# Kernel tuning notes

Hardware: AMD Instinct MI355X
Metric: run time of the kernel (lower is better)

Reference implementation:

```python
import jax, jax.numpy as jnp
import numpy as np
import math

B, L, D = 4, 1024, 1024
H, S = 16, 64
HD = D // H
EPS_LN = 1e-12


def _band_logits_init():
    bl = np.zeros((H, S), dtype=np.float32)
    for h in range(H):
        center = (h + 0.5) * (S / max(H, 1.0))
        for s in range(S):
            dist = s + 0.5 - center
            bl[h, s] = -dist * dist
    return jnp.asarray(bl)


def setup_inputs() -> dict:
    key = jax.random.key(0)
    ks = jax.random.split(key, 12)
    std = 1.0 / math.sqrt(D)
    inp = {
        "hidden_states": jax.random.normal(ks[0], (B, L, D), jnp.float32),
        "attention_mask": jnp.zeros((B, 1, 1, L), jnp.float32),
        "cos_phi": jax.random.normal(ks[1], (B, S, L), jnp.float32),
        "sin_phi": jax.random.normal(ks[2], (B, S, L), jnp.float32),
        "mag": jax.random.uniform(ks[3], (B, S, L), jnp.float32),
        "Wq": jax.random.normal(ks[4], (D, D), jnp.float32) * std,
        "bq": jnp.zeros((D,), jnp.float32),
        "Wk": jax.random.normal(ks[5], (D, D), jnp.float32) * std,
        "bk": jnp.zeros((D,), jnp.float32),
        "Wv": jax.random.normal(ks[6], (D, D), jnp.float32) * std,
        "bv": jnp.zeros((D,), jnp.float32),
        "Wo": jax.random.normal(ks[7], (D, D), jnp.float32) * std,
        "bo": jnp.zeros((D,), jnp.float32),
        "band_logits": _band_logits_init(),
        "phase_bias": jnp.full((H,), 0.5, jnp.float32),
        "gamma": jnp.full((H, S), -3.0, jnp.float32),
        "ln_w": jnp.ones((D,), jnp.float32),
        "ln_b": jnp.zeros((D,), jnp.float32),
    }
    return inp


def _shape_heads(x):
    # [B,L,D] -> [B,H,L,HD]
    return x.reshape(B, L, H, HD).transpose(0, 2, 1, 3)


def reference(hidden_states, attention_mask, cos_phi, sin_phi, mag,
              Wq, bq, Wk, bk, Wv, bv, Wo, bo,
              band_logits, phase_bias, gamma, ln_w, ln_b):
    residual = hidden_states
    q = _shape_heads(hidden_states @ Wq.T + bq)
    k = _shape_heads(hidden_states @ Wk.T + bk)
    v = _shape_heads(hidden_states @ Wv.T + bv)

    cos_pl = cos_phi.transpose(0, 2, 1)  # [B,L,S]
    sin_pl = sin_phi.transpose(0, 2, 1)
    mag_pl = mag.transpose(0, 2, 1)
    mag_pl = mag_pl / (mag_pl.mean(axis=-1, keepdims=True) + 1e-8)

    gamma_pos = jax.nn.softplus(gamma)  # [H,S]
    mag_mix = jnp.tanh(jnp.einsum('bls,hs->bhl', mag_pl, gamma_pos))
    scale = 1.0 + 0.5 * mag_mix[..., None]  # [B,H,L,1]
    q = q * scale
    k = k * scale
    v = v * scale

    attn_scores = jnp.einsum('bhld,bhmd->bhlm', q, k) / math.sqrt(HD)

    band_w_sqrt = jnp.sqrt(jax.nn.softmax(band_logits, axis=-1) + 1e-8)  # [H,S]
    cos_feat = cos_pl[:, None] * band_w_sqrt[None, :, None, :]  # [B,H,L,S]
    sin_feat = sin_pl[:, None] * band_w_sqrt[None, :, None, :]
    phase_align = (jnp.einsum('bhls,bhms->bhlm', cos_feat, cos_feat)
                   + jnp.einsum('bhls,bhms->bhlm', sin_feat, sin_feat)) / math.sqrt(S)

    phase_scale = jax.nn.softplus(phase_bias)[None, :, None, None]
    attn_scores = attn_scores + phase_scale * phase_align + attention_mask

    attn_probs = jax.nn.softmax(attn_scores, axis=-1)
    context = jnp.einsum('bhlm,bhmd->bhld', attn_probs, v)
    context = context.transpose(0, 2, 1, 3).reshape(B, L, D)

    out = context @ Wo.T + bo
    x = out + residual
    mu = x.mean(axis=-1, keepdims=True)
    var = ((x - mu) ** 2).mean(axis=-1, keepdims=True)
    return (x - mu) / jnp.sqrt(var + EPS_LN) * ln_w + ln_b
```

## Files before the change

kernel.cpp:

```cpp
#include <hip/hip_runtime.h>
#include <hip/hip_bf16.h>
#include <math.h>

#define DEV __device__ __forceinline__

typedef __attribute__((ext_vector_type(8))) short short8;
typedef __attribute__((ext_vector_type(8))) unsigned short ushort8v;
typedef __attribute__((ext_vector_type(4))) float f32x4;

DEV unsigned short f2bf(float f) {
  unsigned u = __float_as_uint(f);
  u = u + 0x7fffu + ((u >> 16) & 1u);
  return (unsigned short)(u >> 16);
}

DEV float softplus_f(float x) {
  return (x > 20.f) ? x : log1pf(expf(x));
}

DEV int sw64(int r, int e) { return r * 64 + (e ^ (((r) & 7) << 3)); }
DEV int sw128(int r, int e) { return r * 128 + (e ^ (((r) & 7) << 3)); }

#define GL16(gp, lp) __builtin_amdgcn_global_load_lds( \
    (const __attribute__((address_space(1))) unsigned int*)(gp), \
    (__attribute__((address_space(3))) unsigned int*)(lp), 16, 0, 0)

__global__ __launch_bounds__(256) void k_convall(
    const float* __restrict__ hs, const float* __restrict__ wq,
    const float* __restrict__ wk, const float* __restrict__ wv,
    const float* __restrict__ wo, ushort4* __restrict__ hsb4,
    ushort4* __restrict__ wcat4, ushort4* __restrict__ wob4) {
  const int i = blockIdx.x * 256 + threadIdx.x;
  const float* src;
  ushort4* dst;
  int off;
  if (i < 1048576) {
    src = hs; dst = hsb4; off = i;
  } else {
    const int j = i - 1048576;
    const int g = j >> 18;
    off = j & 262143;
    if (g == 0)      { src = wq; dst = wcat4; }
    else if (g == 1) { src = wk; dst = wcat4 + 262144; }
    else if (g == 2) { src = wv; dst = wcat4 + 524288; }
    else             { src = wo; dst = wob4; }
  }
  const float4 v = reinterpret_cast<const float4*>(src)[off];
  ushort4 o;
  o.x = f2bf(v.x); o.y = f2bf(v.y); o.z = f2bf(v.z); o.w = f2bf(v.w);
  dst[off] = o;
}

__global__ __launch_bounds__(256) void k_prep(
    const float* __restrict__ cos_phi, const float* __restrict__ sin_phi,
    const float* __restrict__ mag, const float* __restrict__ band_logits,
    const float* __restrict__ phase_bias, const float* __restrict__ gamma,
    float* __restrict__ scaleB, unsigned short* __restrict__ feat) {
  const int b = blockIdx.x >> 6;
  const int l0 = ((blockIdx.x >> 2) & 15) << 6;
  const int hq = blockIdx.x & 3;
  const int t = threadIdx.x, lane = t & 63, w = t >> 6;
  __shared__ float cosL[64][65];
  __shared__ float sinL[64][65];
  __shared__ float magL[64][65];
  __shared__ float psum[4][64];
  __shared__ float minv[64];
  __shared__ float bwssL[4][64];
  __shared__ float gposL[4][64];

  {
    const int h = (hq << 2) + w;
    float bl = band_logits[h * 64 + lane];
    float mx = bl;
#pragma unroll
    for (int m = 1; m < 64; m <<= 1) mx = fmaxf(mx, __shfl_xor(mx, m));
    float e = __expf(bl - mx);
    float sm = e;
#pragma unroll
    for (int m = 1; m < 64; m <<= 1) sm += __shfl_xor(sm, m);
    const float ps = softplus_f(phase_bias[h]);
    bwssL[w][lane] = sqrtf(e / sm + 1e-8f) * sqrtf(ps * 0.125f);
    gposL[w][lane] = softplus_f(gamma[h * 64 + lane]);
  }

  const size_t boff = (size_t)b * 65536;
  for (int it = 0; it < 16; ++it) {
    const int s = it * 4 + w, l = lane;
    const size_t g = boff + (size_t)s * 1024 + l0 + l;
    cosL[s][l] = cos_phi[g];
    sinL[s][l] = sin_phi[g];
    magL[s][l] = mag[g];
  }
  __syncthreads();
  {
    const int l = t & 63, g = t >> 6;
    float acc = 0.f;
    for (int i = 0; i < 16; ++i) acc += magL[g * 16 + i][l];
    psum[g][l] = acc;
  }
  __syncthreads();
  if (t < 64) {
    float mean = (psum[0][t] + psum[1][t] + psum[2][t] + psum[3][t]) * (1.f / 64.f);
    minv[t] = 1.f / (mean + 1e-8f);
  }
  __syncthreads();
  {
    const int l = lane;
    const float iv = minv[l];
    const int hidx = (hq << 2) + w;
    float acc = 0.f;
    for (int s = 0; s < 64; ++s) acc += magL[s][l] * gposL[w][s];
    const float tnh = tanhf(acc * iv);
    scaleB[(size_t)(((b << 4) + hidx) << 10) + l0 + l] = 1.f + 0.5f * tnh;
  }
  const int l = t >> 2, sq = (t & 3) << 4;
  for (int hh = 0; hh < 4; ++hh) {
    const int h = (hq << 2) + hh;
    unsigned short* fp = feat + ((size_t)(((b << 4) + h) << 10) + l0 + l) * 128;
    unsigned short cb[16], sb[16];
#pragma unroll
    for (int j = 0; j < 16; ++j) {
      const int s = sq + j;
      const float bw = bwssL[hh][s];
      cb[j] = f2bf(bw * cosL[s][l]);
      sb[j] = f2bf(bw * sinL[s][l]);
    }
    *reinterpret_cast<ushort8v*>(fp + sq) = *reinterpret_cast<ushort8v*>(cb);
    *reinterpret_cast<ushort8v*>(fp + sq + 8) = *reinterpret_cast<ushort8v*>(cb + 8);
    *reinterpret_cast<ushort8v*>(fp + 64 + sq) = *reinterpret_cast<ushort8v*>(sb);
    *reinterpret_cast<ushort8v*>(fp + 64 + sq + 8) = *reinterpret_cast<ushort8v*>(sb + 8);
  }
}

template <int MODE>
__global__ __launch_bounds__(256) void k_gemm(
    const unsigned short* __restrict__ A, const unsigned short* __restrict__ Bt,
    int Ntiles, int K,
    const float* __restrict__ bq, const float* __restrict__ bk,
    const float* __restrict__ bv, const float* __restrict__ scaleB,
    unsigned short* __restrict__ qbuf, unsigned short* __restrict__ kbuf,
    unsigned short* __restrict__ vT,
    const float* __restrict__ bo, const float* __restrict__ resid,
    float* __restrict__ xout) {
  __shared__ __align__(16) short As[128 * 64];
  __shared__ __align__(16) short Bs[128 * 64];
  const int t = threadIdx.x;
  const int lane = t & 63;
  const int w = t >> 6;
  const int cpx = gridDim.x >> 3;
  const int swz = (blockIdx.x & 7) * cpx + (blockIdx.x >> 3);
  const int tm = (swz / Ntiles) << 7;
  const int tn = (swz % Ntiles) << 7;
  const int wR = (w >> 1) << 6;
  const int wC = (w & 1) << 6;
  const int rowS = t >> 3;
  const int offS = (t & 7) << 3;
  const int sgm = (rowS & 7) << 3;
  const int ka = (lane >> 4) << 3;
  const int lm = lane & 15;

  const f32x4 vzero = {0.f, 0.f, 0.f, 0.f};
  f32x4 acc[4][4];
#pragma unroll
  for (int i = 0; i < 4; ++i)
#pragma unroll
    for (int j = 0; j < 4; ++j) acc[i][j] = vzero;

  for (int kt = 0; kt < K; kt += 64) {
    __syncthreads();
#pragma unroll
    for (int p = 0; p < 4; ++p) {
      GL16(A + (size_t)(tm + p * 32 + rowS) * K + kt + (offS ^ sgm), (char*)As + p * 4096 + w * 1024);
      GL16(Bt + (size_t)(tn + p * 32 + rowS) * K + kt + (offS ^ sgm), (char*)Bs + p * 4096 + w * 1024);
    }
    __syncthreads();
    short8 af[4][2], bf[4][2];
#pragma unroll
    for (int mt = 0; mt < 4; ++mt) {
      const int r = wR + mt * 16 + lm;
      af[mt][0] = *(const short8*)&As[sw64(r, ka)];
      af[mt][1] = *(const short8*)&As[sw64(r, 32 + ka)];
    }
#pragma unroll
    for (int nt = 0; nt < 4; ++nt) {
      const int r = wC + nt * 16 + lm;
      bf[nt][0] = *(const short8*)&Bs[sw64(r, ka)];
      bf[nt][1] = *(const short8*)&Bs[sw64(r, 32 + ka)];
    }
#pragma unroll
    for (int mt = 0; mt < 4; ++mt)
#pragma unroll
      for (int nt = 0; nt < 4; ++nt) {
        acc[mt][nt] = __builtin_amdgcn_mfma_f32_16x16x32_bf16(af[mt][0], bf[nt][0], acc[mt][nt], 0, 0, 0);
        acc[mt][nt] = __builtin_amdgcn_mfma_f32_16x16x32_bf16(af[mt][1], bf[nt][1], acc[mt][nt], 0, 0, 0);
      }
  }

#pragma unroll
  for (int mt = 0; mt < 4; ++mt) {
#pragma unroll
    for (int r = 0; r < 4; ++r) {
      const int row = tm + wR + mt * 16 + ((lane >> 4) << 2) + r;
#pragma unroll
      for (int nt = 0; nt < 4; ++nt) {
        const int col = tn + wC + nt * 16 + lm;
        float v = acc[mt][nt][r];
        if (MODE == 0) {
          const int b = row >> 10, l = row & 1023;
          const int sect = col >> 10, jj = col & 1023;
          const int h = jj >> 6, hd = jj & 63;
          const int bh = (b << 4) + h;
          const float sc = scaleB[((size_t)bh << 10) + l];
          if (sect == 0) {
            qbuf[((size_t)bh * 1024 + l) * 64 + hd] = f2bf((v + bq[jj]) * sc * 0.125f);
          } else if (sect == 1) {
            kbuf[((size_t)bh * 1024 + l) * 64 + hd] = f2bf((v + bk[jj]) * sc);
          } else {
            vT[(size_t)bh * 65536 + (size_t)hd * 1024 + l] = f2bf((v + bv[jj]) * sc);
          }
        } else {
          xout[(size_t)row * 1024 + col] = v + bo[col] + resid[(size_t)row * 1024 + col];
        }
      }
    }
  }
}

__global__ __launch_bounds__(256) void k_attn(
    const unsigned short* __restrict__ qbuf, const unsigned short* __restrict__ kbuf,
    const unsigned short* __restrict__ vT, const unsigned short* __restrict__ feat,
    const float* __restrict__ maskg, unsigned short* __restrict__ ctx) {
  __shared__ __align__(16) short Kq[64 * 64];
  __shared__ __align__(16) short Kf[64 * 128];
  __shared__ __align__(16) short Vt[64 * 64];
  __shared__ __align__(16) short Pb[4][16 * 64];

  const int t = threadIdx.x, lane = t & 63, w = t >> 6;
  const int bh = blockIdx.x & 63;
  const int qt = blockIdx.x >> 6;
  const int b = bh >> 4, h = bh & 15;
  const int lm = lane & 15;
  const int ka = (lane >> 4) << 3;

  const int rA = t >> 3, oA = (t & 7) << 3;
  const int rF = t >> 4, oF = (t & 15) << 3;
  const int swA = (rA & 7) << 3;
  const int swF = (rF & 7) << 3;

  const size_t qrow = ((size_t)bh << 10) + qt * 64 + w * 16 + lm;
  short8 aq[2], af[4];
  aq[0] = *(const short8*)(qbuf + qrow * 64 + ka);
  aq[1] = *(const short8*)(qbuf + qrow * 64 + 32 + ka);
#pragma unroll
  for (int kk = 0; kk < 4; ++kk) af[kk] = *(const short8*)(feat + qrow * 128 + kk * 32 + ka);

  short8 ones;
#pragma unroll
  for (int i = 0; i < 8; ++i) ones[i] = (short)0x3F80;

  const f32x4 vzero = {0.f, 0.f, 0.f, 0.f};
  float m_i[4], l_i[4];
  f32x4 o[4];
#pragma unroll
  for (int r = 0; r < 4; ++r) { m_i[r] = -INFINITY; l_i[r] = 0.f; }
#pragma unroll
  for (int nt = 0; nt < 4; ++nt) o[nt] = vzero;

  for (int mt = 0; mt < 16; ++mt) {
    __syncthreads();
#pragma unroll
    for (int p = 0; p < 2; ++p) {
      GL16(kbuf + (((size_t)bh << 10) + mt * 64 + p * 32 + rA) * 64 + (oA ^ swA),
           (char*)Kq + p * 4096 + w * 1024);
      GL16(vT + ((size_t)bh << 16) + (size_t)(p * 32 + rA) * 1024 + mt * 64 + (oA ^ swA),
           (char*)Vt + p * 4096 + w * 1024);
    }
#pragma unroll
    for (int p = 0; p < 4; ++p) {
      GL16(feat + (((size_t)bh << 10) + mt * 64 + p * 16 + rF) * 128 + (oF ^ swF),
           (char*)Kf + p * 4096 + w * 1024);
    }
    float mk[4];
#pragma unroll
    for (int nt = 0; nt < 4; ++nt) mk[nt] = maskg[(b << 10) + mt * 64 + nt * 16 + lm];
    __syncthreads();

    f32x4 s[4];
#pragma unroll
    for (int nt = 0; nt < 4; ++nt) s[nt] = vzero;
#pragma unroll
    for (int nt = 0; nt < 4; ++nt) {
      const int rk = nt * 16 + lm;
      s[nt] = __builtin_amdgcn_mfma_f32_16x16x32_bf16(aq[0], *(const short8*)&Kq[sw64(rk, ka)], s[nt], 0, 0, 0);
      s[nt] = __builtin_amdgcn_mfma_f32_16x16x32_bf16(aq[1], *(const short8*)&Kq[sw64(rk, 32 + ka)], s[nt], 0, 0, 0);
#pragma unroll
      for (int kk = 0; kk < 4; ++kk)
        s[nt] = __builtin_amdgcn_mfma_f32_16x16x32_bf16(af[kk], *(const short8*)&Kf[sw128(rk, kk * 32 + ka)], s[nt], 0, 0, 0);
    }

    float pmax[4], al[4];
#pragma unroll
    for (int r = 0; r < 4; ++r) {
      float v0 = fmaxf(fmaxf(s[0][r] + mk[0], s[1][r] + mk[1]),
                       fmaxf(s[2][r] + mk[2], s[3][r] + mk[3]));
#pragma unroll
      for (int m = 1; m < 16; m <<= 1) v0 = fmaxf(v0, __shfl_xor(v0, m));
      pmax[r] = v0;
    }
    int need = 0;
#pragma unroll
    for (int r = 0; r < 4; ++r) need |= (pmax[r] > m_i[r] + 8.f) ? 1 : 0;
    if (__any(need)) {
#pragma unroll
      for (int r = 0; r < 4; ++r) {
        const float mnew = fmaxf(m_i[r], pmax[r]);
        al[r] = __expf(m_i[r] - mnew);
        m_i[r] = mnew;
      }
#pragma unroll
      for (int nt = 0; nt < 4; ++nt)
#pragma unroll
        for (int r = 0; r < 4; ++r) o[nt][r] *= al[r];
    } else {
#pragma unroll
      for (int r = 0; r < 4; ++r) al[r] = 1.f;
    }
#pragma unroll
    for (int nt = 0; nt < 4; ++nt)
#pragma unroll
      for (int r = 0; r < 4; ++r)
        s[nt][r] = __expf(s[nt][r] + mk[nt] - m_i[r]);

    short* Pw = &Pb[w][0];
#pragma unroll
    for (int nt = 0; nt < 4; ++nt)
#pragma unroll
      for (int r = 0; r < 4; ++r) {
        const int prow = ((lane >> 4) << 2) + r;
        Pw[sw64(prow, nt * 16 + lm)] = (short)f2bf(s[nt][r]);
      }

    short8 ap0 = *(const short8*)&Pw[sw64(lm, ka)];
    short8 ap1 = *(const short8*)&Pw[sw64(lm, 32 + ka)];

    f32x4 rs = vzero;
    rs = __builtin_amdgcn_mfma_f32_16x16x32_bf16(ap0, ones, rs, 0, 0, 0);
    rs = __builtin_amdgcn_mfma_f32_16x16x32_bf16(ap1, ones, rs, 0, 0, 0);

#pragma unroll
    for (int nt = 0; nt < 4; ++nt) {
      const int rv = nt * 16 + lm;
      o[nt] = __builtin_amdgcn_mfma_f32_16x16x32_bf16(ap0, *(const short8*)&Vt[sw64(rv, ka)], o[nt], 0, 0, 0);
      o[nt] = __builtin_amdgcn_mfma_f32_16x16x32_bf16(ap1, *(const short8*)&Vt[sw64(rv, 32 + ka)], o[nt], 0, 0, 0);
    }

#pragma unroll
    for (int r = 0; r < 4; ++r) l_i[r] = l_i[r] * al[r] + rs[r];
  }

#pragma unroll
  for (int r = 0; r < 4; ++r) {
    const float inv = 1.f / l_i[r];
    const int row = (b << 10) + qt * 64 + w * 16 + ((lane >> 4) << 2) + r;
#pragma unroll
    for (int nt = 0; nt < 4; ++nt) {
      const int col = (h << 6) + nt * 16 + lm;
      ctx[(size_t)row * 1024 + col] = (short)f2bf(o[nt][r] * inv);
    }
  }
}

__global__ __launch_bounds__(256) void k_ln(const float* __restrict__ x,
                                            const float* __restrict__ lw,
                                            const float* __restrict__ lb,
                                            float* __restrict__ out) {
  const int row = blockIdx.x, t = threadIdx.x, lane = t & 63, w = t >> 6;
  const float4 v = reinterpret_cast<const float4*>(x + (size_t)row * 1024)[t];
  float s = v.x + v.y + v.z + v.w;
  float s2 = v.x * v.x + v.y * v.y + v.z * v.z + v.w * v.w;
#pragma unroll
  for (int m = 1; m < 64; m <<= 1) {
    s += __shfl_xor(s, m);
    s2 += __shfl_xor(s2, m);
  }
  __shared__ float rs[4], rs2[4];
  if (lane == 0) { rs[w] = s; rs2[w] = s2; }
  __syncthreads();
  const float S = rs[0] + rs[1] + rs[2] + rs[3];
  const float S2 = rs2[0] + rs2[1] + rs2[2] + rs2[3];
  const float mu = S * (1.f / 1024.f);
  const float var = fmaxf(S2 * (1.f / 1024.f) - mu * mu, 0.f);
  const float rstd = rsqrtf(var + 1e-12f);
  const float4 wv = reinterpret_cast<const float4*>(lw)[t];
  const float4 bv = reinterpret_cast<const float4*>(lb)[t];
  float4 o;
  o.x = (v.x - mu) * rstd * wv.x + bv.x;
  o.y = (v.y - mu) * rstd * wv.y + bv.y;
  o.z = (v.z - mu) * rstd * wv.z + bv.z;
  o.w = (v.w - mu) * rstd * wv.w + bv.w;
  reinterpret_cast<float4*>(out + (size_t)row * 1024)[t] = o;
}

extern "C" void kernel_launch(void* const* d_in, const int* in_sizes, int n_in,
                              void* d_out, int out_size, void* d_ws, size_t ws_size,
                              hipStream_t stream) {
  const float* hs = (const float*)d_in[0];
  const float* mask = (const float*)d_in[1];
  const float* cosp = (const float*)d_in[2];
  const float* sinp = (const float*)d_in[3];
  const float* mag = (const float*)d_in[4];
  const float* Wq = (const float*)d_in[5];
  const float* bq = (const float*)d_in[6];
  const float* Wk = (const float*)d_in[7];
  const float* bk = (const float*)d_in[8];
  const float* Wv = (const float*)d_in[9];
  const float* bv = (const float*)d_in[10];
  const float* Wo = (const float*)d_in[11];
  const float* bo = (const float*)d_in[12];
  const float* bl = (const float*)d_in[13];
  const float* pb = (const float*)d_in[14];
  const float* gm = (const float*)d_in[15];
  const float* lw = (const float*)d_in[16];
  const float* lbv = (const float*)d_in[17];
  float* outp = (float*)d_out;

  char* ws = (char*)d_ws;
  unsigned short* hsb  = (unsigned short*)(ws);
  unsigned short* wcat = (unsigned short*)(ws + 8388608);
  unsigned short* wob  = (unsigned short*)(ws + 14680064);
  unsigned short* qbuf = (unsigned short*)(ws + 16777216);
  unsigned short* kbuf = (unsigned short*)(ws + 25165824);
  unsigned short* vT   = (unsigned short*)(ws + 33554432);
  unsigned short* feat = (unsigned short*)(ws + 41943040);
  unsigned short* ctx  = (unsigned short*)(ws + 58720256);
  float* scaleB = (float*)(ws + 67108864);
  float* xbuf   = (float*)(ws + 16777216);

  k_convall<<<8192, 256, 0, stream>>>(hs, Wq, Wk, Wv, Wo, (ushort4*)hsb,
                                      (ushort4*)wcat, (ushort4*)wob);
  k_prep<<<256, 256, 0, stream>>>(cosp, sinp, mag, bl, pb, gm, scaleB, feat);
  k_gemm<0><<<32 * 24, 256, 0, stream>>>(hsb, wcat, 24, 1024, bq, bk, bv, scaleB,
                                         qbuf, kbuf, vT, nullptr, nullptr, nullptr);
  k_attn<<<1024, 256, 0, stream>>>(qbuf, kbuf, vT, feat, mask, ctx);
  k_gemm<1><<<32 * 8, 256, 0, stream>>>(ctx, wob, 8, 1024, nullptr, nullptr, nullptr,
                                        nullptr, nullptr, nullptr, nullptr, bo, hs, xbuf);
  k_ln<<<4096, 256, 0, stream>>>(xbuf, lw, lbv, outp);
}
```

Before: 183.6 us.

## Rework attention kernel around 32x32 MFMA with 128-row query tiles

Rewrites the attention kernel so each wave handles 32 query rows with 32x32x16 bf16 MFMAs, computing S^T = K·Q^T so each lane owns one query row. Row max and sum now need one cross-half shuffle, and the ones-MFMA row sum is dropped. The block covers 128 queries, which halves the grid and doubles K/V/feature reuse per LDS load. The mask is staged once in LDS, P and the output are packed with v_cvt_pk_bf16_f32, and context is written back with coalesced 16-byte stores through LDS. The cost is more LDS per block, more accumulator registers and fewer blocks, which may lower occupancy.

```diff
diff --git a/kernel.cpp b/kernel.cpp
--- a/kernel.cpp
+++ b/kernel.cpp
@@ -7,6 +7,7 @@
 typedef __attribute__((ext_vector_type(8))) short short8;
 typedef __attribute__((ext_vector_type(8))) unsigned short ushort8v;
 typedef __attribute__((ext_vector_type(4))) float f32x4;
+typedef __attribute__((ext_vector_type(16))) float f32x16;
 
 DEV unsigned short f2bf(float f) {
   unsigned u = __float_as_uint(f);
@@ -14,12 +15,19 @@
   return (unsigned short)(u >> 16);
 }
 
+DEV unsigned cvtpk(float a, float b) {
+  unsigned r;
+  asm("v_cvt_pk_bf16_f32 %0, %1, %2" : "=v"(r) : "v"(a), "v"(b));
+  return r;
+}
+
 DEV float softplus_f(float x) {
   return (x > 20.f) ? x : log1pf(expf(x));
 }
 
 DEV int sw64(int r, int e) { return r * 64 + (e ^ (((r) & 7) << 3)); }
 DEV int sw128(int r, int e) { return r * 128 + (e ^ (((r) & 7) << 3)); }
+DEV int swKf(int r, int e) { return r * 128 + (e ^ (((r) & 15) << 3)); }
 
 #define GL16(gp, lp) __builtin_amdgcn_global_load_lds( \
     (const __attribute__((address_space(1))) unsigned int*)(gp), \
@@ -233,140 +241,173 @@
   __shared__ __align__(16) short Kq[64 * 64];
   __shared__ __align__(16) short Kf[64 * 128];
   __shared__ __align__(16) short Vt[64 * 64];
-  __shared__ __align__(16) short Pb[4][16 * 64];
+  __shared__ __align__(16) short Pb[4][32 * 64];
+  __shared__ float maskS[1024];
 
   const int t = threadIdx.x, lane = t & 63, w = t >> 6;
   const int bh = blockIdx.x & 63;
   const int qt = blockIdx.x >> 6;
   const int b = bh >> 4, h = bh & 15;
-  const int lm = lane & 15;
-  const int ka = (lane >> 4) << 3;
+  const int l31 = lane & 31;
+  const int hi = lane >> 5;
 
   const int rA = t >> 3, oA = (t & 7) << 3;
   const int rF = t >> 4, oF = (t & 15) << 3;
-  const int swA = (rA & 7) << 3;
-  const int swF = (rF & 7) << 3;
-
-  const size_t qrow = ((size_t)bh << 10) + qt * 64 + w * 16 + lm;
-  short8 aq[2], af[4];
-  aq[0] = *(const short8*)(qbuf + qrow * 64 + ka);
-  aq[1] = *(const short8*)(qbuf + qrow * 64 + 32 + ka);
-#pragma unroll
-  for (int kk = 0; kk < 4; ++kk) af[kk] = *(const short8*)(feat + qrow * 128 + kk * 32 + ka);
-
-  short8 ones;
-#pragma unroll
-  for (int i = 0; i < 8; ++i) ones[i] = (short)0x3F80;
-
-  const f32x4 vzero = {0.f, 0.f, 0.f, 0.f};
-  float m_i[4], l_i[4];
-  f32x4 o[4];
-#pragma unroll
-  for (int r = 0; r < 4; ++r) { m_i[r] = -INFINITY; l_i[r] = 0.f; }
-#pragma unroll
-  for (int nt = 0; nt < 4; ++nt) o[nt] = vzero;
+
+  reinterpret_cast<float4*>(maskS)[t] =
+      reinterpret_cast<const float4*>(maskg + ((size_t)b << 10))[t];
+
+  const size_t qrow = ((size_t)bh << 10) + qt * 128 + w * 32 + l31;
+  short8 qf[12];
+#pragma unroll
+  for (int ks = 0; ks < 4; ++ks)
+    qf[ks] = *(const short8*)(qbuf + qrow * 64 + ks * 16 + hi * 8);
+#pragma unroll
+  for (int ks = 4; ks < 12; ++ks)
+    qf[ks] = *(const short8*)(feat + qrow * 128 + (ks - 4) * 16 + hi * 8);
+
+  f32x16 o0, o1;
+#pragma unroll
+  for (int r = 0; r < 16; ++r) { o0[r] = 0.f; o1[r] = 0.f; }
+  float m_i = -INFINITY, l_i = 0.f;
 
   for (int mt = 0; mt < 16; ++mt) {
     __syncthreads();
 #pragma unroll
     for (int p = 0; p < 2; ++p) {
-      GL16(kbuf + (((size_t)bh << 10) + mt * 64 + p * 32 + rA) * 64 + (oA ^ swA),
+      const int rr = rA + 32 * p;
+      GL16(kbuf + (((size_t)bh << 10) + mt * 64 + rr) * 64 + (oA ^ ((rr & 7) << 3)),
            (char*)Kq + p * 4096 + w * 1024);
-      GL16(vT + ((size_t)bh << 16) + (size_t)(p * 32 + rA) * 1024 + mt * 64 + (oA ^ swA),
+      GL16(vT + ((size_t)bh << 16) + (size_t)rr * 1024 + mt * 64 + (oA ^ ((rr & 7) << 3)),
            (char*)Vt + p * 4096 + w * 1024);
     }
 #pragma unroll
     for (int p = 0; p < 4; ++p) {
-      GL16(feat + (((size_t)bh << 10) + mt * 64 + p * 16 + rF) * 128 + (oF ^ swF),
+      const int rr = rF + 16 * p;
+      GL16(feat + (((size_t)bh << 10) + mt * 64 + rr) * 128 + (oF ^ ((rr & 15) << 3)),
            (char*)Kf + p * 4096 + w * 1024);
     }
-    float mk[4];
-#pragma unroll
-    for (int nt = 0; nt < 4; ++nt) mk[nt] = maskg[(b << 10) + mt * 64 + nt * 16 + lm];
     __syncthreads();
 
-    f32x4 s[4];
-#pragma unroll
-    for (int nt = 0; nt < 4; ++nt) s[nt] = vzero;
-#pragma unroll
-    for (int nt = 0; nt < 4; ++nt) {
-      const int rk = nt * 16 + lm;
-      s[nt] = __builtin_amdgcn_mfma_f32_16x16x32_bf16(aq[0], *(const short8*)&Kq[sw64(rk, ka)], s[nt], 0, 0, 0);
-      s[nt] = __builtin_amdgcn_mfma_f32_16x16x32_bf16(aq[1], *(const short8*)&Kq[sw64(rk, 32 + ka)], s[nt], 0, 0, 0);
-#pragma unroll
-      for (int kk = 0; kk < 4; ++kk)
-        s[nt] = __builtin_amdgcn_mfma_f32_16x16x32_bf16(af[kk], *(const short8*)&Kf[sw128(rk, kk * 32 + ka)], s[nt], 0, 0, 0);
-    }
-
-    float pmax[4], al[4];
-#pragma unroll
-    for (int r = 0; r < 4; ++r) {
-      float v0 = fmaxf(fmaxf(s[0][r] + mk[0], s[1][r] + mk[1]),
-                       fmaxf(s[2][r] + mk[2], s[3][r] + mk[3]));
-#pragma unroll
-      for (int m = 1; m < 16; m <<= 1) v0 = fmaxf(v0, __shfl_xor(v0, m));
-      pmax[r] = v0;
-    }
-    int need = 0;
-#pragma unroll
-    for (int r = 0; r < 4; ++r) need |= (pmax[r] > m_i[r] + 8.f) ? 1 : 0;
-    if (__any(need)) {
-#pragma unroll
-      for (int r = 0; r < 4; ++r) {
-        const float mnew = fmaxf(m_i[r], pmax[r]);
-        al[r] = __expf(m_i[r] - mnew);
-        m_i[r] = mnew;
+    f32x16 s0, s1;
+#pragma unroll
+    for (int r = 0; r < 16; ++r) { s0[r] = 0.f; s1[r] = 0.f; }
+#pragma unroll
+    for (int ks = 0; ks < 4; ++ks) {
+      const int C = ks * 16 + hi * 8;
+      short8 a0 = *(const short8*)&Kq[sw64(l31, C)];
+      short8 a1 = *(const short8*)&Kq[sw64(32 + l31, C)];
+      s0 = __builtin_amdgcn_mfma_f32_32x32x16_bf16(a0, qf[ks], s0, 0, 0, 0);
+      s1 = __builtin_amdgcn_mfma_f32_32x32x16_bf16(a1, qf[ks], s1, 0, 0, 0);
+    }
+#pragma unroll
+    for (int ks = 4; ks < 12; ++ks) {
+      const int C = (ks - 4) * 16 + hi * 8;
+      short8 a0 = *(const short8*)&Kf[swKf(l31, C)];
+      short8 a1 = *(const short8*)&Kf[swKf(32 + l31, C)];
+      s0 = __builtin_amdgcn_mfma_f32_32x32x16_bf16(a0, qf[ks], s0, 0, 0, 0);
+      s1 = __builtin_amdgcn_mfma_f32_32x32x16_bf16(a1, qf[ks], s1, 0, 0, 0);
+    }
+
+#pragma unroll
+    for (int j = 0; j < 4; ++j) {
+      const float4 mk0 = *(const float4*)&maskS[mt * 64 + j * 8 + hi * 4];
+      const float4 mk1 = *(const float4*)&maskS[mt * 64 + 32 + j * 8 + hi * 4];
+      s0[4 * j + 0] += mk0.x; s0[4 * j + 1] += mk0.y;
+      s0[4 * j + 2] += mk0.z; s0[4 * j + 3] += mk0.w;
+      s1[4 * j + 0] += mk1.x; s1[4 * j + 1] += mk1.y;
+      s1[4 * j + 2] += mk1.z; s1[4 * j + 3] += mk1.w;
+    }
+
+    float mx8[8];
+#pragma unroll
+    for (int i = 0; i < 8; ++i)
+      mx8[i] = fmaxf(fmaxf(s0[i], s0[i + 8]), fmaxf(s1[i], s1[i + 8]));
+    float pm = fmaxf(fmaxf(fmaxf(mx8[0], mx8[1]), fmaxf(mx8[2], mx8[3])),
+                     fmaxf(fmaxf(mx8[4], mx8[5]), fmaxf(mx8[6], mx8[7])));
+    pm = fmaxf(pm, __shfl_xor(pm, 32));
+
+    float al = 1.f;
+    if (__any(pm > m_i + 8.f)) {
+      const float mnew = fmaxf(m_i, pm);
+      al = __expf(m_i - mnew);
+      m_i = mnew;
+#pragma unroll
+      for (int r = 0; r < 16; ++r) { o0[r] *= al; o1[r] *= al; }
+    }
+
+#pragma unroll
+    for (int r = 0; r < 16; ++r) {
+      s0[r] = __expf(s0[r] - m_i);
+      s1[r] = __expf(s1[r] - m_i);
+    }
+
+    float sm8[8];
+#pragma unroll
+    for (int i = 0; i < 8; ++i) sm8[i] = (s0[i] + s0[i + 8]) + (s1[i] + s1[i + 8]);
+    float sm = ((sm8[0] + sm8[1]) + (sm8[2] + sm8[3])) +
+               ((sm8[4] + sm8[5]) + (sm8[6] + sm8[7]));
+    sm += __shfl_xor(sm, 32);
+    l_i = l_i * al + sm;
+
+    short* Pw = &Pb[w][0];
+#pragma unroll
+    for (int j = 0; j < 4; ++j) {
+      {
+        const int K0 = j * 8 + hi * 4;
+        uint2 d;
+        d.x = cvtpk(s0[4 * j + 0], s0[4 * j + 1]);
+        d.y = cvtpk(s0[4 * j + 2], s0[4 * j + 3]);
+        *(uint2*)&Pw[l31 * 64 + (K0 ^ ((l31 & 7) << 3))] = d;
       }
-#pragma unroll
-      for (int nt = 0; nt < 4; ++nt)
-#pragma unroll
-        for (int r = 0; r < 4; ++r) o[nt][r] *= al[r];
-    } else {
-#pragma unroll
-      for (int r = 0; r < 4; ++r) al[r] = 1.f;
-    }
-#pragma unroll
-    for (int nt = 0; nt < 4; ++nt)
-#pragma unroll
-      for (int r = 0; r < 4; ++r)
-        s[nt][r] = __expf(s[nt][r] + mk[nt] - m_i[r]);
-
-    short* Pw = &Pb[w][0];
-#pragma unroll
-    for (int nt = 0; nt < 4; ++nt)
-#pragma unroll
-      for (int r = 0; r < 4; ++r) {
-        const int prow = ((lane >> 4) << 2) + r;
-        Pw[sw64(prow, nt * 16 + lm)] = (short)f2bf(s[nt][r]);
+      {
+        const int K0 = 32 + j * 8 + hi * 4;
+        uint2 d;
+        d.x = cvtpk(s1[4 * j + 0], s1[4 * j + 1]);
+        d.y = cvtpk(s1[4 * j + 2], s1[4 * j + 3]);
+        *(uint2*)&Pw[l31 * 64 + (K0 ^ ((l31 & 7) << 3))] = d;
       }
-
-    short8 ap0 = *(const short8*)&Pw[sw64(lm, ka)];
-    short8 ap1 = *(const short8*)&Pw[sw64(lm, 32 + ka)];
-
-    f32x4 rs = vzero;
-    rs = __builtin_amdgcn_mfma_f32_16x16x32_bf16(ap0, ones, rs, 0, 0, 0);
-    rs = __builtin_amdgcn_mfma_f32_16x16x32_bf16(ap1, ones, rs, 0, 0, 0);
-
-#pragma unroll
-    for (int nt = 0; nt < 4; ++nt) {
-      const int rv = nt * 16 + lm;
-      o[nt] = __builtin_amdgcn_mfma_f32_16x16x32_bf16(ap0, *(const short8*)&Vt[sw64(rv, ka)], o[nt], 0, 0, 0);
-      o[nt] = __builtin_amdgcn_mfma_f32_16x16x32_bf16(ap1, *(const short8*)&Vt[sw64(rv, 32 + ka)], o[nt], 0, 0, 0);
-    }
-
-#pragma unroll
-    for (int r = 0; r < 4; ++r) l_i[r] = l_i[r] * al[r] + rs[r];
-  }
-
-#pragma unroll
-  for (int r = 0; r < 4; ++r) {
-    const float inv = 1.f / l_i[r];
-    const int row = (b << 10) + qt * 64 + w * 16 + ((lane >> 4) << 2) + r;
-#pragma unroll
-    for (int nt = 0; nt < 4; ++nt) {
-      const int col = (h << 6) + nt * 16 + lm;
-      ctx[(size_t)row * 1024 + col] = (short)f2bf(o[nt][r] * inv);
-    }
+    }
+
+#pragma unroll
+    for (int ks2 = 0; ks2 < 4; ++ks2) {
+      const int C = ks2 * 16 + hi * 8;
+      short8 pf = *(const short8*)&Pw[l31 * 64 + (C ^ ((l31 & 7) << 3))];
+      short8 v0 = *(const short8*)&Vt[sw64(l31, C)];
+      short8 v1 = *(const short8*)&Vt[sw64(32 + l31, C)];
+      o0 = __builtin_amdgcn_mfma_f32_32x32x16_bf16(v0, pf, o0, 0, 0, 0);
+      o1 = __builtin_amdgcn_mfma_f32_32x32x16_bf16(v1, pf, o1, 0, 0, 0);
+    }
+  }
+
+  const float inv = 1.f / l_i;
+#pragma unroll
+  for (int r = 0; r < 16; ++r) { o0[r] *= inv; o1[r] *= inv; }
+  short* Pw = &Pb[w][0];
+#pragma unroll
+  for (int j = 0; j < 4; ++j) {
+    {
+      const int D0 = j * 8 + hi * 4;
+      uint2 d;
+      d.x = cvtpk(o0[4 * j + 0], o0[4 * j + 1]);
+      d.y = cvtpk(o0[4 * j + 2], o0[4 * j + 3]);
+      *(uint2*)&Pw[l31 * 64 + (D0 ^ ((l31 & 7) << 3))] = d;
+    }
+    {
+      const int D0 = 32 + j * 8 + hi * 4;
+      uint2 d;
+      d.x = cvtpk(o1[4 * j + 0], o1[4 * j + 1]);
+      d.y = cvtpk(o1[4 * j + 2], o1[4 * j + 3]);
+      *(uint2*)&Pw[l31 * 64 + (D0 ^ ((l31 & 7) << 3))] = d;
+    }
+  }
+  const int qq = lane >> 3, ch = lane & 7;
+#pragma unroll
+  for (int p = 0; p < 4; ++p) {
+    const int q2 = p * 8 + qq;
+    const uint4 vv = *(const uint4*)&Pw[q2 * 64 + ((ch * 8) ^ ((q2 & 7) << 3))];
+    const size_t row = ((size_t)b << 10) + qt * 128 + w * 32 + q2;
+    *(uint4*)&ctx[row * 1024 + h * 64 + ch * 8] = vv;
   }
 }
 
@@ -441,7 +482,7 @@
   k_prep<<<256, 256, 0, stream>>>(cosp, sinp, mag, bl, pb, gm, scaleB, feat);
   k_gemm<0><<<32 * 24, 256, 0, stream>>>(hsb, wcat, 24, 1024, bq, bk, bv, scaleB,
                                          qbuf, kbuf, vT, nullptr, nullptr, nullptr);
-  k_attn<<<1024, 256, 0, stream>>>(qbuf, kbuf, vT, feat, mask, ctx);
+  k_attn<<<512, 256, 0, stream>>>(qbuf, kbuf, vT, feat, mask, ctx);
   k_gemm<1><<<32 * 8, 256, 0, stream>>>(ctx, wob, 8, 1024, nullptr, nullptr, nullptr,
                                         nullptr, nullptr, nullptr, nullptr, bo, hs, xbuf);
   k_ln<<<4096, 256, 0, stream>>>(xbuf, lw, lbv, outp);
```

New measurement: 153.1 us. 16.6% less time.
